# Optimization experiments

Hardware: AMD Instinct MI355X
Metric: run time of the kernel (lower is better)

## Reference

```python
import jax, jax.numpy as jnp
import numpy as np

NUM_C = 1000
B, L = 8, 1024
D, H, NB, DFF = 512, 8, 4, 2048
DK = D // H
EPS = 1e-5


def _ln(x, s, b):
    mu = jnp.mean(x, axis=-1, keepdims=True)
    var = jnp.mean((x - mu) ** 2, axis=-1, keepdims=True)
    return (x - mu) * jax.lax.rsqrt(var + EPS) * s + b


def setup_inputs() -> dict:
    key = jax.random.key(0)
    ks = iter(jax.random.split(key, 64))

    def nrm(shape, scale=0.02):
        return jax.random.normal(next(ks), shape, dtype=jnp.float32) * scale

    inp = {
        "q": jax.random.randint(next(ks), (B, L), 0, NUM_C),
        "r": jax.random.randint(next(ks), (B, L), 0, 2),
        # embeddings
        "ctx_emb": nrm((NUM_C * 2, D)),
        "val_emb": nrm((NUM_C * 2, D)),
        "skill_emb": nrm((NUM_C, D)),
        "pos_emb": nrm((L, D)),
        # attention projections, stacked over blocks
        "Wq": nrm((NB, D, D)), "bq": jnp.zeros((NB, D)),
        "Wk": nrm((NB, D, D)), "bk": jnp.zeros((NB, D)),
        "Wv": nrm((NB, D, D)), "bv": jnp.zeros((NB, D)),
        "Wo": nrm((NB, D, D)), "bo": jnp.zeros((NB, D)),
        # layer norms (ctx / val streams, pre- and post-FFN)
        "ln1c_s": jnp.ones((NB, D)), "ln1c_b": jnp.zeros((NB, D)),
        "ln1v_s": jnp.ones((NB, D)), "ln1v_b": jnp.zeros((NB, D)),
        "ln2c_s": jnp.ones((NB, D)), "ln2c_b": jnp.zeros((NB, D)),
        "ln2v_s": jnp.ones((NB, D)), "ln2v_b": jnp.zeros((NB, D)),
        # FFNs
        "fc1c_W": nrm((NB, D, DFF)), "fc1c_b": jnp.zeros((NB, DFF)),
        "fc2c_W": nrm((NB, DFF, D)), "fc2c_b": jnp.zeros((NB, D)),
        "fc1v_W": nrm((NB, D, DFF)), "fc1v_b": jnp.zeros((NB, DFF)),
        "fc2v_W": nrm((NB, DFF, D)), "fc2v_b": jnp.zeros((NB, D)),
        # prediction head: [3D -> DFF -> 256 -> 1]
        "hW1": nrm((3 * D, DFF)), "hb1": jnp.zeros((DFF,)),
        "hW2": nrm((DFF, 256)), "hb2": jnp.zeros((256,)),
        "hW3": nrm((256, 1)), "hb3": jnp.zeros((1,)),
    }
    return inp


def reference(q, r, ctx_emb, val_emb, skill_emb, pos_emb,
              Wq, bq, Wk, bk, Wv, bv, Wo, bo,
              ln1c_s, ln1c_b, ln1v_s, ln1v_b,
              ln2c_s, ln2c_b, ln2v_s, ln2v_b,
              fc1c_W, fc1c_b, fc2c_W, fc2c_b,
              fc1v_W, fc1v_b, fc2v_W, fc2v_b,
              hW1, hb1, hW2, hb2, hW3, hb3):
    inter = q + NUM_C * r                       # [B, L] interaction ids
    pos = pos_emb[None, :L, :]
    ctx = ctx_emb[inter] + pos                  # [B, L, D]
    val = val_emb[inter] + pos                  # [B, L, D]
    causal = jnp.tril(jnp.ones((L, L), dtype=bool))
    scale = 1.0 / (DK ** 0.5)

    for i in range(NB):
        # dual-stream MHA: Q,K from ctx; V from val
        Q = (ctx @ Wq[i] + bq[i]).reshape(B, L, H, DK)
        K = (ctx @ Wk[i] + bk[i]).reshape(B, L, H, DK)
        V = (val @ Wv[i] + bv[i]).reshape(B, L, H, DK)
        # fp32 scores (as in torch source), mask==0 -> -inf, softmax
        scores = jnp.einsum('bqhd,bkhd->bhqk', Q.astype(jnp.float32),
                            K.astype(jnp.float32)) * scale
        scores = jnp.where(causal, scores, -jnp.inf)
        attn = jax.nn.softmax(scores, axis=-1)  # dropout = identity (eval)
        out = jnp.einsum('bhqk,bkhd->bqhd', attn, V).reshape(B, L, D)
        out = out @ Wo[i] + bo[i]
        # shared attn output added to both streams, separate norms
        ctx = _ln(ctx + out, ln1c_s[i], ln1c_b[i])
        val = _ln(val + out, ln1v_s[i], ln1v_b[i])
        # dual FFNs
        f_ctx = jax.nn.relu(ctx @ fc1c_W[i] + fc1c_b[i]) @ fc2c_W[i] + fc2c_b[i]
        ctx = _ln(ctx + f_ctx, ln2c_s[i], ln2c_b[i])
        f_val = jax.nn.relu(val @ fc1v_W[i] + fc1v_b[i]) @ fc2v_W[i] + fc2v_b[i]
        val = _ln(val + f_val, ln2v_s[i], ln2v_b[i])

    feat = jnp.concatenate([ctx, val, skill_emb[q]], axis=-1)  # [B, L, 3D]
    h = jax.nn.relu(feat @ hW1 + hb1)
    h = jax.nn.relu(h @ hW2 + hb2)
    logits = (h @ hW3 + hb3)[..., 0]
    return jax.nn.sigmoid(logits)               # [B, L] p(correct)
```

## Files before the change

### kernel.cpp

```cpp
#include <hip/hip_runtime.h>
#include <hip/hip_bf16.h>
#include <math.h>

#define TOK 8192
#define DM 512
#define NH 8
#define DKH 64
#define DFFN 2048
#define SEQ 1024
#define NBLK 4
#define NUMC 1000

typedef __attribute__((ext_vector_type(8))) short bf16x8;
typedef __attribute__((ext_vector_type(4))) float f32x4;
typedef __attribute__((ext_vector_type(4))) ushort u16x4;
typedef __hip_bfloat16 bf16;

__device__ __forceinline__ void gload_lds16(const ushort* g, ushort* l) {
    __builtin_amdgcn_global_load_lds(
        (const __attribute__((address_space(1))) void*)g,
        (__attribute__((address_space(3))) void*)l, 16, 0, 0);
}

__global__ __launch_bounds__(256) void embed_kernel(
    const int* __restrict__ q, const int* __restrict__ r,
    const float* __restrict__ ctx_emb, const float* __restrict__ val_emb,
    const float* __restrict__ pos_emb,
    float* __restrict__ ctx32, float* __restrict__ val32,
    bf16* __restrict__ ctx16, bf16* __restrict__ val16)
{
    const int t = blockIdx.x;
    const int inter = q[t] + NUMC * r[t];
    const int l = t & (SEQ - 1);
    const float* ce = ctx_emb + (size_t)inter * DM;
    const float* ve = val_emb + (size_t)inter * DM;
    const float* pe = pos_emb + (size_t)l * DM;
    const size_t o = (size_t)t * DM;
    for (int d = threadIdx.x; d < DM; d += 256) {
        float p = pe[d];
        float c = ce[d] + p;
        float v = ve[d] + p;
        ctx32[o + d] = c; val32[o + d] = v;
        ctx16[o + d] = __float2bfloat16(c);
        val16[o + d] = __float2bfloat16(v);
    }
}

__global__ __launch_bounds__(256) void transpose_kernel(
    const float* __restrict__ src, bf16* __restrict__ dst,
    int K, int N, long sb, long db)
{
    __shared__ float t[32][33];
    src += (long)blockIdx.z * sb;
    dst += (long)blockIdx.z * db;
    const int n0 = blockIdx.x * 32;
    const int k0 = blockIdx.y * 32;
    const int tx = threadIdx.x;
    const int ty = threadIdx.y;
    for (int i = ty; i < 32; i += 8) t[i][tx] = src[(size_t)(k0 + i) * N + n0 + tx];
    __syncthreads();
    for (int i = ty; i < 32; i += 8)
        dst[(size_t)(n0 + i) * K + k0 + tx] = __float2bfloat16(t[tx][i]);
}

template<int BN, bool OUTBF16>
__global__ __launch_bounds__(256, 3) void mfma_gemm(
    const ushort* __restrict__ A, const ushort* __restrict__ Bt,
    const float* __restrict__ bias1, const float* __restrict__ bias2, int split,
    void* __restrict__ Cv, int N, int K, int relu, int vtmode,
    const ushort* __restrict__ A1, const ushort* __restrict__ Bt1,
    const float* __restrict__ bias1_1, void* __restrict__ Cv1)
{
    if (blockIdx.z) { A = A1; Bt = Bt1; bias1 = bias1_1; Cv = Cv1; }
    constexpr int MI = (BN == 128) ? 4 : 2;
    constexpr int BR = BN / 32;
    __shared__ ushort As[128 * 64];
    __shared__ ushort Bs[BN * 64];
    const int tid = threadIdx.x;
    const int wave = tid >> 6;
    const int lane = tid & 63;
    const int ln = lane & 15;
    const int kq = lane >> 4;
    const int nx = gridDim.x;
    const int lin = blockIdx.x + nx * blockIdx.y;
    const int loc = lin >> 3;
    const int mdiv = loc / nx;
    const int bm = ((lin & 7) + 8 * mdiv) * 128;
    const int bn = (loc - mdiv * nx) * BN;
    const int wr = (BN == 128) ? (wave >> 1) * 64 : wave * 32;
    const int wc = (BN == 128) ? (wave & 1) * 64 : 0;

    const int trow = tid >> 3;
    const int gcb = (tid & 7) ^ (trow & 7);
    const ushort* Ab = A + (size_t)(bm + trow) * K + gcb * 8;
    const ushort* Bb = Bt + (size_t)(bn + trow) * K + gcb * 8;
    ushort* AsW = As + wave * 512;
    ushort* BsW = Bs + wave * 512;

    f32x4 acc[MI][4];
#pragma unroll
    for (int i = 0; i < MI; ++i)
#pragma unroll
        for (int j = 0; j < 4; ++j) acc[i][j] = (f32x4){0.f, 0.f, 0.f, 0.f};

    for (int k0 = 0; k0 < K; k0 += 64) {
        __syncthreads();
#pragma unroll
        for (int p = 0; p < 4; ++p)
            gload_lds16(Ab + (size_t)32 * p * K + k0, AsW + p * 2048);
#pragma unroll
        for (int p = 0; p < BR; ++p)
            gload_lds16(Bb + (size_t)32 * p * K + k0, BsW + p * 2048);
        __syncthreads();
#pragma unroll
        for (int half = 0; half < 2; ++half) {
            const int cb = ((half * 4 + kq) ^ (ln & 7)) * 8;
            bf16x8 bfr[4];
#pragma unroll
            for (int j = 0; j < 4; ++j)
                bfr[j] = *(const bf16x8*)&Bs[(wc + j * 16 + ln) * 64 + cb];
#pragma unroll
            for (int i = 0; i < MI; ++i) {
                const bf16x8 af = *(const bf16x8*)&As[(wr + i * 16 + ln) * 64 + cb];
#pragma unroll
                for (int j = 0; j < 4; ++j)
                    acc[i][j] = __builtin_amdgcn_mfma_f32_16x16x32_bf16(af, bfr[j], acc[i][j], 0, 0, 0);
            }
        }
    }

#pragma unroll
    for (int i = 0; i < MI; ++i) {
        const int rowb = bm + wr + i * 16 + kq * 4;
#pragma unroll
        for (int j = 0; j < 4; ++j) {
            const int colg = bn + wc + j * 16 + ln;
            const float bv = (colg < split) ? bias1[colg] : bias2[colg - split];
            if (vtmode) {
                union { u16x4 v; ushort u[4]; } pk;
#pragma unroll
                for (int rr = 0; rr < 4; ++rr) {
                    float v = acc[i][j][rr] + bv;
                    bf16 t = __float2bfloat16(v);
                    pk.u[rr] = *(ushort*)&t;
                }
                *(u16x4*)((ushort*)Cv + ((size_t)(rowb >> 10) * 512 + colg) * 1024 + (rowb & 1023)) = pk.v;
            } else {
#pragma unroll
                for (int rr = 0; rr < 4; ++rr) {
                    float v = acc[i][j][rr] + bv;
                    if (relu) v = fmaxf(v, 0.f);
                    if (OUTBF16)
                        ((bf16*)Cv)[(size_t)(rowb + rr) * N + colg] = __float2bfloat16(v);
                    else
                        ((float*)Cv)[(size_t)(rowb + rr) * N + colg] = v;
                }
            }
        }
    }
}

__global__ __launch_bounds__(256) void attn_kernel(
    const bf16* __restrict__ QK, const bf16* __restrict__ Vt,
    bf16* __restrict__ Og)
{
    __shared__ ushort Qs[64 * 64];
    __shared__ ushort Ks[64 * 64];
    __shared__ ushort Vs[64 * 64];
    __shared__ ushort Ps[4 * 16 * 68];

    const int tid = threadIdx.x;
    const int wave = tid >> 6, lane = tid & 63;
    const int ln = lane & 15, kq = lane >> 4;
    const int lin = blockIdx.x + 16 * blockIdx.y;
    const int loc = lin >> 3;
    const int qt = loc & 15;
    const int bh = (lin & 7) + 8 * (loc >> 4);
    const int b = bh >> 3, h = bh & 7;

    const int srow = tid >> 3;
    const int sgcb = (tid & 7) ^ (srow & 7);
    const ushort* gQ = (const ushort*)QK + (size_t)(b * SEQ + qt * 64 + srow) * 1024 + h * 64 + sgcb * 8;
    const ushort* gK = (const ushort*)QK + (size_t)(b * SEQ + srow) * 1024 + 512 + h * 64 + sgcb * 8;
    const ushort* gV = (const ushort*)Vt + (size_t)(bh * 64 + srow) * 1024 + sgcb * 8;
    ushort* QsW = Qs + wave * 512;
    ushort* KsW = Ks + wave * 512;
    ushort* VsW = Vs + wave * 512;

    gload_lds16(gQ, QsW);
    gload_lds16(gQ + 32 * 1024, QsW + 2048);

    float rs[4];
    f32x4 oacc[4];
#pragma unroll
    for (int r = 0; r < 4; ++r) { rs[r] = 0.f; oacc[r] = (f32x4){0.f, 0.f, 0.f, 0.f}; }
    const float sc2 = 0.125f * 1.4426950408889634f;

    const int cb0 = (kq ^ (ln & 7)) * 8;
    const int cb1 = ((4 + kq) ^ (ln & 7)) * 8;

    for (int kt = 0; kt <= qt; ++kt) {
        __syncthreads();
        gload_lds16(gK + (size_t)kt * 64 * 1024, KsW);
        gload_lds16(gK + (size_t)(kt * 64 + 32) * 1024, KsW + 2048);
        gload_lds16(gV + kt * 64, VsW);
        gload_lds16(gV + 32 * 1024 + kt * 64, VsW + 2048);
        __syncthreads();

        const bf16x8 aq0 = *(const bf16x8*)&Qs[(wave * 16 + ln) * 64 + cb0];
        const bf16x8 aq1 = *(const bf16x8*)&Qs[(wave * 16 + ln) * 64 + cb1];
        f32x4 s[4];
#pragma unroll
        for (int c = 0; c < 4; ++c) {
            const bf16x8 bk0 = *(const bf16x8*)&Ks[(c * 16 + ln) * 64 + cb0];
            const bf16x8 bk1 = *(const bf16x8*)&Ks[(c * 16 + ln) * 64 + cb1];
            s[c] = (f32x4){0.f, 0.f, 0.f, 0.f};
            s[c] = __builtin_amdgcn_mfma_f32_16x16x32_bf16(aq0, bk0, s[c], 0, 0, 0);
            s[c] = __builtin_amdgcn_mfma_f32_16x16x32_bf16(aq1, bk1, s[c], 0, 0, 0);
        }
        if (kt == qt) {
#pragma unroll
            for (int c = 0; c < 4; ++c)
#pragma unroll
                for (int r = 0; r < 4; ++r) {
                    const int qg = wave * 16 + kq * 4 + r;
                    const int jg = c * 16 + ln;
                    const float pv = (jg <= qg) ? exp2f(s[c][r] * sc2) : 0.f;
                    rs[r] += pv;
                    *(bf16*)&Ps[wave * 1088 + (kq * 4 + r) * 68 + c * 16 + ln] = __float2bfloat16(pv);
                }
        } else {
#pragma unroll
            for (int c = 0; c < 4; ++c)
#pragma unroll
                for (int r = 0; r < 4; ++r) {
                    const float pv = exp2f(s[c][r] * sc2);
                    rs[r] += pv;
                    *(bf16*)&Ps[wave * 1088 + (kq * 4 + r) * 68 + c * 16 + ln] = __float2bfloat16(pv);
                }
        }
        const bf16x8 ap0 = *(const bf16x8*)&Ps[wave * 1088 + ln * 68 + kq * 8];
        const bf16x8 ap1 = *(const bf16x8*)&Ps[wave * 1088 + ln * 68 + 32 + kq * 8];
#pragma unroll
        for (int c2 = 0; c2 < 4; ++c2) {
            const bf16x8 bv0 = *(const bf16x8*)&Vs[(c2 * 16 + ln) * 64 + cb0];
            const bf16x8 bv1 = *(const bf16x8*)&Vs[(c2 * 16 + ln) * 64 + cb1];
            oacc[c2] = __builtin_amdgcn_mfma_f32_16x16x32_bf16(ap0, bv0, oacc[c2], 0, 0, 0);
            oacc[c2] = __builtin_amdgcn_mfma_f32_16x16x32_bf16(ap1, bv1, oacc[c2], 0, 0, 0);
        }
    }
    float inv[4];
#pragma unroll
    for (int r = 0; r < 4; ++r) {
        float v = rs[r];
        v += __shfl_xor(v, 1);
        v += __shfl_xor(v, 2);
        v += __shfl_xor(v, 4);
        v += __shfl_xor(v, 8);
        inv[r] = 1.f / v;
    }
#pragma unroll
    for (int c2 = 0; c2 < 4; ++c2)
#pragma unroll
        for (int r = 0; r < 4; ++r)
            Og[(size_t)(b * SEQ + qt * 64 + wave * 16 + kq * 4 + r) * 512 + h * 64 + c2 * 16 + ln]
                = __float2bfloat16(oacc[c2][r] * inv[r]);
}

__global__ __launch_bounds__(256) void lnp_kernel(
    const float* __restrict__ x0, const bf16* __restrict__ r0, const float* __restrict__ s0,
    const float* __restrict__ b0, float* __restrict__ of0, bf16* __restrict__ oh0,
    const float* __restrict__ x1, const bf16* __restrict__ r1, const float* __restrict__ s1,
    const float* __restrict__ b1, float* __restrict__ of1, bf16* __restrict__ oh1)
{
    const float* x = x0; const bf16* res = r0; const float* s = s0; const float* bb = b0;
    float* of = of0; bf16* oh = oh0;
    if (blockIdx.y) { x = x1; res = r1; s = s1; bb = b1; of = of1; oh = oh1; }
    __shared__ float w1[4], w2[4];
    const size_t o = (size_t)blockIdx.x * DM;
    const int i0 = threadIdx.x, i1 = threadIdx.x + 256;
    const float v0 = x[o + i0] + __bfloat162float(res[o + i0]);
    const float v1 = x[o + i1] + __bfloat162float(res[o + i1]);
    float sum = v0 + v1;
#pragma unroll
    for (int off = 32; off; off >>= 1) sum += __shfl_down(sum, off);
    if ((threadIdx.x & 63) == 0) w1[threadIdx.x >> 6] = sum;
    __syncthreads();
    const float mu = (w1[0] + w1[1] + w1[2] + w1[3]) * (1.f / DM);
    const float d0 = v0 - mu, d1 = v1 - mu;
    float vs = d0 * d0 + d1 * d1;
#pragma unroll
    for (int off = 32; off; off >>= 1) vs += __shfl_down(vs, off);
    if ((threadIdx.x & 63) == 0) w2[threadIdx.x >> 6] = vs;
    __syncthreads();
    const float rstd = rsqrtf((w2[0] + w2[1] + w2[2] + w2[3]) * (1.f / DM) + 1e-5f);
    const float o0 = d0 * rstd * s[i0] + bb[i0];
    const float o1 = d1 * rstd * s[i1] + bb[i1];
    of[o + i0] = o0; of[o + i1] = o1;
    oh[o + i0] = __float2bfloat16(o0);
    oh[o + i1] = __float2bfloat16(o1);
}

__global__ __launch_bounds__(256) void gather_kernel(
    const bf16* __restrict__ ctx16, const bf16* __restrict__ val16,
    const float* __restrict__ skill, const int* __restrict__ q,
    bf16* __restrict__ feat)
{
    const int t = blockIdx.x;
    const float* sp = skill + (size_t)q[t] * DM;
    const bf16* cp = ctx16 + (size_t)t * DM;
    const bf16* vp = val16 + (size_t)t * DM;
    bf16* fp = feat + (size_t)t * (3 * DM);
    for (int d = threadIdx.x; d < DM; d += 256) {
        fp[d] = cp[d];
        fp[DM + d] = vp[d];
        fp[2 * DM + d] = __float2bfloat16(sp[d]);
    }
}

__global__ __launch_bounds__(256) void logits_kernel(
    const float* __restrict__ h2, const float* __restrict__ w,
    const float* __restrict__ bptr, float* __restrict__ out)
{
    __shared__ float w1[4];
    const int t = blockIdx.x;
    float sum = h2[(size_t)t * 256 + threadIdx.x] * w[threadIdx.x];
#pragma unroll
    for (int off = 32; off; off >>= 1) sum += __shfl_down(sum, off);
    if ((threadIdx.x & 63) == 0) w1[threadIdx.x >> 6] = sum;
    __syncthreads();
    if (threadIdx.x == 0) {
        const float logit = w1[0] + w1[1] + w1[2] + w1[3] + bptr[0];
        out[t] = 1.f / (1.f + __expf(-logit));
    }
}

extern "C" void kernel_launch(void* const* d_in, const int* in_sizes, int n_in,
                              void* d_out, int out_size, void* d_ws, size_t ws_size,
                              hipStream_t stream)
{
    const int*   q         = (const int*)d_in[0];
    const int*   r         = (const int*)d_in[1];
    const float* ctx_emb   = (const float*)d_in[2];
    const float* val_emb   = (const float*)d_in[3];
    const float* skill_emb = (const float*)d_in[4];
    const float* pos_emb   = (const float*)d_in[5];
    const float* Wq = (const float*)d_in[6];
    const float* bq = (const float*)d_in[7];
    const float* Wk = (const float*)d_in[8];
    const float* bk = (const float*)d_in[9];
    const float* Wv = (const float*)d_in[10];
    const float* bv = (const float*)d_in[11];
    const float* Wo = (const float*)d_in[12];
    const float* bo = (const float*)d_in[13];
    const float* ln1c_s = (const float*)d_in[14];
    const float* ln1c_b = (const float*)d_in[15];
    const float* ln1v_s = (const float*)d_in[16];
    const float* ln1v_b = (const float*)d_in[17];
    const float* ln2c_s = (const float*)d_in[18];
    const float* ln2c_b = (const float*)d_in[19];
    const float* ln2v_s = (const float*)d_in[20];
    const float* ln2v_b = (const float*)d_in[21];
    const float* fc1c_W = (const float*)d_in[22];
    const float* fc1c_b = (const float*)d_in[23];
    const float* fc2c_W = (const float*)d_in[24];
    const float* fc2c_b = (const float*)d_in[25];
    const float* fc1v_W = (const float*)d_in[26];
    const float* fc1v_b = (const float*)d_in[27];
    const float* fc2v_W = (const float*)d_in[28];
    const float* fc2v_b = (const float*)d_in[29];
    const float* hW1 = (const float*)d_in[30];
    const float* hb1 = (const float*)d_in[31];
    const float* hW2 = (const float*)d_in[32];
    const float* hb2 = (const float*)d_in[33];
    const float* hW3 = (const float*)d_in[34];
    const float* hb3 = (const float*)d_in[35];
    float* out = (float*)d_out;

    char* p = (char*)d_ws;
    auto alloc = [&](size_t bytes) { char* ret = p; p += bytes; return ret; };
    float* ctx32 = (float*)alloc(16777216);
    float* val32 = (float*)alloc(16777216);
    bf16*  ob16c = (bf16*)alloc(8388608);
    bf16*  ob16v = (bf16*)alloc(8388608);
    bf16*  ctx16 = (bf16*)alloc(8388608);
    bf16*  val16 = (bf16*)alloc(8388608);
    bf16*  qk16  = (bf16*)alloc(16777216);
    bf16*  v16pad= (bf16*)alloc(8388608);
    bf16*  vt16  = (bf16*)alloc(8388608);
    bf16*  att16 = (bf16*)alloc(8388608);
    bf16*  mid16c = (bf16*)alloc(33554432);
    bf16*  qkT   = (bf16*)alloc(4194304);
    bf16*  vT    = (bf16*)alloc(2097152);
    bf16*  oT    = (bf16*)alloc(2097152);
    bf16*  fc1cT = (bf16*)alloc(8388608);
    bf16*  fc2cT = (bf16*)alloc(8388608);
    bf16*  fc1vT = (bf16*)alloc(8388608);
    bf16*  fc2vT = (bf16*)alloc(8388608);
    bf16*  hW1T  = (bf16*)alloc(6291456);
    bf16*  hW2T  = (bf16*)alloc(1048576);
    (void)v16pad;
    bf16*  mid16v = qk16;
    bf16*  feat16 = qk16;
    float* h2     = (float*)vt16;

    const dim3 tb(32, 8);
    transpose_kernel<<<dim3(16, 16, 4), tb, 0, stream>>>(Wq, qkT,          512, 512, 262144, 524288);
    transpose_kernel<<<dim3(16, 16, 4), tb, 0, stream>>>(Wk, qkT + 262144, 512, 512, 262144, 524288);
    transpose_kernel<<<dim3(16, 16, 4), tb, 0, stream>>>(Wv, vT, 512, 512, 262144, 262144);
    transpose_kernel<<<dim3(16, 16, 4), tb, 0, stream>>>(Wo, oT, 512, 512, 262144, 262144);
    transpose_kernel<<<dim3(64, 16, 4), tb, 0, stream>>>(fc1c_W, fc1cT, 512, 2048, 1048576, 1048576);
    transpose_kernel<<<dim3(16, 64, 4), tb, 0, stream>>>(fc2c_W, fc2cT, 2048, 512, 1048576, 1048576);
    transpose_kernel<<<dim3(64, 16, 4), tb, 0, stream>>>(fc1v_W, fc1vT, 512, 2048, 1048576, 1048576);
    transpose_kernel<<<dim3(16, 64, 4), tb, 0, stream>>>(fc2v_W, fc2vT, 2048, 512, 1048576, 1048576);
    transpose_kernel<<<dim3(64, 48, 1), tb, 0, stream>>>(hW1, hW1T, 1536, 2048, 0, 0);
    transpose_kernel<<<dim3(8, 64, 1),  tb, 0, stream>>>(hW2, hW2T, 2048, 256, 0, 0);

    embed_kernel<<<TOK, 256, 0, stream>>>(q, r, ctx_emb, val_emb, pos_emb,
                                          ctx32, val32, ctx16, val16);

    for (int i = 0; i < NBLK; ++i) {
        mfma_gemm<128, true><<<dim3(8, 64), 256, 0, stream>>>(
            (const ushort*)ctx16, (const ushort*)(qkT + (size_t)i * 524288),
            bq + i * DM, bk + i * DM, 512, qk16, 1024, 512, 0, 0,
            nullptr, nullptr, nullptr, nullptr);
        mfma_gemm<64, true><<<dim3(8, 64), 256, 0, stream>>>(
            (const ushort*)val16, (const ushort*)(vT + (size_t)i * 262144),
            bv + i * DM, nullptr, 1 << 30, vt16, 512, 512, 0, 1,
            nullptr, nullptr, nullptr, nullptr);
        attn_kernel<<<dim3(16, 64), 256, 0, stream>>>(qk16, vt16, att16);
        mfma_gemm<64, true><<<dim3(8, 64), 256, 0, stream>>>(
            (const ushort*)att16, (const ushort*)(oT + (size_t)i * 262144),
            bo + i * DM, nullptr, 1 << 30, ob16c, 512, 512, 0, 0,
            nullptr, nullptr, nullptr, nullptr);
        lnp_kernel<<<dim3(TOK, 2), 256, 0, stream>>>(
            ctx32, ob16c, ln1c_s + i * DM, ln1c_b + i * DM, ctx32, ctx16,
            val32, ob16c, ln1v_s + i * DM, ln1v_b + i * DM, val32, val16);
        mfma_gemm<128, true><<<dim3(16, 64, 2), 256, 0, stream>>>(
            (const ushort*)ctx16, (const ushort*)(fc1cT + (size_t)i * 1048576),
            fc1c_b + i * DFFN, nullptr, 1 << 30, mid16c, 2048, 512, 1, 0,
            (const ushort*)val16, (const ushort*)(fc1vT + (size_t)i * 1048576),
            fc1v_b + i * DFFN, mid16v);
        mfma_gemm<128, true><<<dim3(4, 64, 2), 256, 0, stream>>>(
            (const ushort*)mid16c, (const ushort*)(fc2cT + (size_t)i * 1048576),
            fc2c_b + i * DM, nullptr, 1 << 30, ob16c, 512, 2048, 0, 0,
            (const ushort*)mid16v, (const ushort*)(fc2vT + (size_t)i * 1048576),
            fc2v_b + i * DM, ob16v);
        lnp_kernel<<<dim3(TOK, 2), 256, 0, stream>>>(
            ctx32, ob16c, ln2c_s + i * DM, ln2c_b + i * DM, ctx32, ctx16,
            val32, ob16v, ln2v_s + i * DM, ln2v_b + i * DM, val32, val16);
    }

    gather_kernel<<<TOK, 256, 0, stream>>>(ctx16, val16, skill_emb, q, feat16);
    mfma_gemm<128, true><<<dim3(16, 64), 256, 0, stream>>>(
        (const ushort*)feat16, (const ushort*)hW1T, hb1, nullptr, 1 << 30, mid16c, 2048, 1536, 1, 0,
        nullptr, nullptr, nullptr, nullptr);
    mfma_gemm<64, false><<<dim3(4, 64), 256, 0, stream>>>(
        (const ushort*)mid16c, (const ushort*)hW2T, hb2, nullptr, 1 << 30, h2, 256, 2048, 1, 0,
        nullptr, nullptr, nullptr, nullptr);
    logits_kernel<<<TOK, 256, 0, stream>>>(h2, hW3, hb3, out);
}
```

Baseline: 1.120 ms.

## Add 256x256-tile double-buffered MFMA GEMM for FC1 and head GEMMs

Introduces a new 512-thread GEMM kernel with 256x256 output tiles, double-buffered LDS staging via global_load_lds, XOR-swizzled LDS layout, grouped block ordering and setprio around MFMA bursts. It replaces the 128-tile GEMM for the dual FC1 projections and the first head layer. Larger tiles raise arithmetic intensity and cut global reloads, and overlapping the next tile load with compute hides latency. In exchange it uses more LDS per block and fewer blocks, which lowers occupancy and wave balance.

```diff
diff --git a/kernel.cpp b/kernel.cpp
--- a/kernel.cpp
+++ b/kernel.cpp
@@ -20,6 +20,12 @@
     __builtin_amdgcn_global_load_lds(
         (const __attribute__((address_space(1))) void*)g,
         (__attribute__((address_space(3))) void*)l, 16, 0, 0);
+}
+
+__device__ __forceinline__ void wgbar() {
+    asm volatile("" ::: "memory");
+    __builtin_amdgcn_s_barrier();
+    asm volatile("" ::: "memory");
 }
 
 __global__ __launch_bounds__(256) void embed_kernel(
@@ -155,6 +161,111 @@
                     else
                         ((float*)Cv)[(size_t)(rowb + rr) * N + colg] = v;
                 }
+            }
+        }
+    }
+}
+
+__device__ __forceinline__ void stage256(const ushort* Ag, const ushort* Bg,
+                                         ushort* AsD, ushort* BsD, int K, int kk)
+{
+#pragma unroll
+    for (int p = 0; p < 4; ++p)
+        gload_lds16(Ag + (size_t)(64 * p) * K + kk, AsD + p * 4096);
+#pragma unroll
+    for (int p = 0; p < 4; ++p)
+        gload_lds16(Bg + (size_t)(64 * p) * K + kk, BsD + p * 4096);
+}
+
+__global__ __launch_bounds__(512, 2) void mfma_gemm256(
+    const ushort* __restrict__ A, const ushort* __restrict__ Bt,
+    const float* __restrict__ bias, bf16* __restrict__ C, int N, int K, int relu,
+    const ushort* __restrict__ A1, const ushort* __restrict__ Bt1,
+    const float* __restrict__ bias1, bf16* __restrict__ C1)
+{
+    if (blockIdx.z) { A = A1; Bt = Bt1; bias = bias1; C = C1; }
+    __shared__ ushort As[2 * 16384];
+    __shared__ ushort Bs[2 * 16384];
+    const int tid = threadIdx.x;
+    const int wave = tid >> 6, lane = tid & 63;
+    const int ln = lane & 15, kq = lane >> 4;
+    const int wr = wave >> 2;
+    const int wc = wave & 3;
+
+    const int nx = gridDim.x;
+    const int lin = blockIdx.x + nx * blockIdx.y;
+    const int loc = lin >> 3;
+    const int mdiv = loc / nx;
+    const int bm = ((lin & 7) + 8 * mdiv) * 256;
+    const int bn = (loc - mdiv * nx) * 256;
+
+    const int srow = tid >> 3;
+    const int sgcb = (tid & 7) ^ (srow & 7);
+    const ushort* Ag = A + (size_t)(bm + srow) * K + sgcb * 8;
+    const ushort* Bg = Bt + (size_t)(bn + srow) * K + sgcb * 8;
+    const int wofs = wave * 512;
+
+    f32x4 acc[8][4];
+#pragma unroll
+    for (int i = 0; i < 8; ++i)
+#pragma unroll
+        for (int j = 0; j < 4; ++j) acc[i][j] = (f32x4){0.f, 0.f, 0.f, 0.f};
+
+    const int NT = K >> 6;
+    stage256(Ag, Bg, As + wofs, Bs + wofs, K, 0);
+
+    for (int t = 0; t < NT; ++t) {
+        const int b = t & 1;
+        const int k0 = t << 6;
+        if (t + 1 < NT) {
+            stage256(Ag, Bg, As + (b ^ 1) * 16384 + wofs, Bs + (b ^ 1) * 16384 + wofs, K, k0 + 64);
+            asm volatile("s_waitcnt vmcnt(8)" ::: "memory");
+        } else {
+            asm volatile("s_waitcnt vmcnt(0)" ::: "memory");
+        }
+        wgbar();
+
+        const ushort* Asb = As + b * 16384;
+        const ushort* Bsb = Bs + b * 16384;
+        bf16x8 bf[4][2];
+#pragma unroll
+        for (int j = 0; j < 4; ++j)
+#pragma unroll
+            for (int h = 0; h < 2; ++h)
+                bf[j][h] = *(const bf16x8*)&Bsb[(wc * 64 + j * 16 + ln) * 64 + (((h * 4 + kq) ^ (ln & 7)) * 8)];
+#pragma unroll
+        for (int q = 0; q < 4; ++q) {
+            bf16x8 af0[2], af1[2];
+#pragma unroll
+            for (int h = 0; h < 2; ++h) {
+                af0[h] = *(const bf16x8*)&Asb[(wr * 128 + (2 * q) * 16 + ln) * 64 + (((h * 4 + kq) ^ (ln & 7)) * 8)];
+                af1[h] = *(const bf16x8*)&Asb[(wr * 128 + (2 * q + 1) * 16 + ln) * 64 + (((h * 4 + kq) ^ (ln & 7)) * 8)];
+            }
+            __builtin_amdgcn_s_setprio(1);
+#pragma unroll
+            for (int h = 0; h < 2; ++h)
+#pragma unroll
+                for (int j = 0; j < 4; ++j) {
+                    acc[2 * q][j]     = __builtin_amdgcn_mfma_f32_16x16x32_bf16(af0[h], bf[j][h], acc[2 * q][j], 0, 0, 0);
+                    acc[2 * q + 1][j] = __builtin_amdgcn_mfma_f32_16x16x32_bf16(af1[h], bf[j][h], acc[2 * q + 1][j], 0, 0, 0);
+                }
+            __builtin_amdgcn_s_setprio(0);
+            wgbar();
+        }
+    }
+
+#pragma unroll
+    for (int i = 0; i < 8; ++i) {
+        const int gr = bm + wr * 128 + i * 16 + kq * 4;
+#pragma unroll
+        for (int j = 0; j < 4; ++j) {
+            const int gc = bn + wc * 64 + j * 16 + ln;
+            const float bv = bias[gc];
+#pragma unroll
+            for (int rr = 0; rr < 4; ++rr) {
+                float v = acc[i][j][rr] + bv;
+                if (relu) v = fmaxf(v, 0.f);
+                C[(size_t)(gr + rr) * N + gc] = __float2bfloat16(v);
             }
         }
     }
@@ -436,9 +547,9 @@
         lnp_kernel<<<dim3(TOK, 2), 256, 0, stream>>>(
             ctx32, ob16c, ln1c_s + i * DM, ln1c_b + i * DM, ctx32, ctx16,
             val32, ob16c, ln1v_s + i * DM, ln1v_b + i * DM, val32, val16);
-        mfma_gemm<128, true><<<dim3(16, 64, 2), 256, 0, stream>>>(
+        mfma_gemm256<<<dim3(8, 32, 2), 512, 0, stream>>>(
             (const ushort*)ctx16, (const ushort*)(fc1cT + (size_t)i * 1048576),
-            fc1c_b + i * DFFN, nullptr, 1 << 30, mid16c, 2048, 512, 1, 0,
+            fc1c_b + i * DFFN, mid16c, 2048, 512, 1,
             (const ushort*)val16, (const ushort*)(fc1vT + (size_t)i * 1048576),
             fc1v_b + i * DFFN, mid16v);
         mfma_gemm<128, true><<<dim3(4, 64, 2), 256, 0, stream>>>(
@@ -452,8 +563,8 @@
     }
 
     gather_kernel<<<TOK, 256, 0, stream>>>(ctx16, val16, skill_emb, q, feat16);
-    mfma_gemm<128, true><<<dim3(16, 64), 256, 0, stream>>>(
-        (const ushort*)feat16, (const ushort*)hW1T, hb1, nullptr, 1 << 30, mid16c, 2048, 1536, 1, 0,
+    mfma_gemm256<<<dim3(8, 32), 512, 0, stream>>>(
+        (const ushort*)feat16, (const ushort*)hW1T, hb1, mid16c, 2048, 1536, 1,
         nullptr, nullptr, nullptr, nullptr);
     mfma_gemm<64, false><<<dim3(4, 64), 256, 0, stream>>>(
         (const ushort*)mid16c, (const ushort*)hW2T, hb2, nullptr, 1 << 30, h2, 256, 2048, 1, 0,
```

After: 1.140 ms. Within noise of the previous version (+1.8%).

## Double-buffer K/V tiles in attention kernel with async prefetch

Applied to the files above, without the earlier changes.

Double-buffers the K and V shared-memory tiles in the causal attention kernel. The next tile is prefetched with direct global-to-LDS loads while the current one is computed, and explicit vmcnt waits plus raw barriers replace the two __syncthreads per iteration. The aim is to hide global-load latency behind MFMA work. It also raises wave priority around the MFMA sections, and it doubles K/V shared-memory use, which may reduce occupancy.

```diff
diff --git a/kernel.cpp b/kernel.cpp
--- a/kernel.cpp
+++ b/kernel.cpp
@@ -20,6 +20,12 @@
     __builtin_amdgcn_global_load_lds(
         (const __attribute__((address_space(1))) void*)g,
         (__attribute__((address_space(3))) void*)l, 16, 0, 0);
+}
+
+__device__ __forceinline__ void wgbar() {
+    asm volatile("" ::: "memory");
+    __builtin_amdgcn_s_barrier();
+    asm volatile("" ::: "memory");
 }
 
 __global__ __launch_bounds__(256) void embed_kernel(
@@ -165,8 +171,8 @@
     bf16* __restrict__ Og)
 {
     __shared__ ushort Qs[64 * 64];
-    __shared__ ushort Ks[64 * 64];
-    __shared__ ushort Vs[64 * 64];
+    __shared__ ushort Ks[2][64 * 64];
+    __shared__ ushort Vs[2][64 * 64];
     __shared__ ushort Ps[4 * 16 * 68];
 
     const int tid = threadIdx.x;
@@ -184,12 +190,17 @@
     const ushort* gK = (const ushort*)QK + (size_t)(b * SEQ + srow) * 1024 + 512 + h * 64 + sgcb * 8;
     const ushort* gV = (const ushort*)Vt + (size_t)(bh * 64 + srow) * 1024 + sgcb * 8;
     ushort* QsW = Qs + wave * 512;
-    ushort* KsW = Ks + wave * 512;
-    ushort* VsW = Vs + wave * 512;
 
     gload_lds16(gQ, QsW);
     gload_lds16(gQ + 32 * 1024, QsW + 2048);
 
+    {
+        gload_lds16(gK, Ks[0] + wave * 512);
+        gload_lds16(gK + (size_t)32 * 1024, Ks[0] + 2048 + wave * 512);
+        gload_lds16(gV, Vs[0] + wave * 512);
+        gload_lds16(gV + (size_t)32 * 1024, Vs[0] + 2048 + wave * 512);
+    }
+
     float rs[4];
     f32x4 oacc[4];
 #pragma unroll
@@ -200,24 +211,33 @@
     const int cb1 = ((4 + kq) ^ (ln & 7)) * 8;
 
     for (int kt = 0; kt <= qt; ++kt) {
-        __syncthreads();
-        gload_lds16(gK + (size_t)kt * 64 * 1024, KsW);
-        gload_lds16(gK + (size_t)(kt * 64 + 32) * 1024, KsW + 2048);
-        gload_lds16(gV + kt * 64, VsW);
-        gload_lds16(gV + 32 * 1024 + kt * 64, VsW + 2048);
-        __syncthreads();
+        const int bf = kt & 1;
+        wgbar();
+        if (kt < qt) {
+            const size_t kn = (size_t)(kt + 1) * 64;
+            gload_lds16(gK + kn * 1024, Ks[bf ^ 1] + wave * 512);
+            gload_lds16(gK + (kn + 32) * 1024, Ks[bf ^ 1] + 2048 + wave * 512);
+            gload_lds16(gV + kn, Vs[bf ^ 1] + wave * 512);
+            gload_lds16(gV + (size_t)32 * 1024 + kn, Vs[bf ^ 1] + 2048 + wave * 512);
+            asm volatile("s_waitcnt vmcnt(4)" ::: "memory");
+        } else {
+            asm volatile("s_waitcnt vmcnt(0)" ::: "memory");
+        }
+        wgbar();
 
         const bf16x8 aq0 = *(const bf16x8*)&Qs[(wave * 16 + ln) * 64 + cb0];
         const bf16x8 aq1 = *(const bf16x8*)&Qs[(wave * 16 + ln) * 64 + cb1];
         f32x4 s[4];
+        __builtin_amdgcn_s_setprio(1);
 #pragma unroll
         for (int c = 0; c < 4; ++c) {
-            const bf16x8 bk0 = *(const bf16x8*)&Ks[(c * 16 + ln) * 64 + cb0];
-            const bf16x8 bk1 = *(const bf16x8*)&Ks[(c * 16 + ln) * 64 + cb1];
+            const bf16x8 bk0 = *(const bf16x8*)&Ks[bf][(c * 16 + ln) * 64 + cb0];
+            const bf16x8 bk1 = *(const bf16x8*)&Ks[bf][(c * 16 + ln) * 64 + cb1];
             s[c] = (f32x4){0.f, 0.f, 0.f, 0.f};
             s[c] = __builtin_amdgcn_mfma_f32_16x16x32_bf16(aq0, bk0, s[c], 0, 0, 0);
             s[c] = __builtin_amdgcn_mfma_f32_16x16x32_bf16(aq1, bk1, s[c], 0, 0, 0);
         }
+        __builtin_amdgcn_s_setprio(0);
         if (kt == qt) {
 #pragma unroll
             for (int c = 0; c < 4; ++c)
@@ -241,13 +261,15 @@
         }
         const bf16x8 ap0 = *(const bf16x8*)&Ps[wave * 1088 + ln * 68 + kq * 8];
         const bf16x8 ap1 = *(const bf16x8*)&Ps[wave * 1088 + ln * 68 + 32 + kq * 8];
+        __builtin_amdgcn_s_setprio(1);
 #pragma unroll
         for (int c2 = 0; c2 < 4; ++c2) {
-            const bf16x8 bv0 = *(const bf16x8*)&Vs[(c2 * 16 + ln) * 64 + cb0];
-            const bf16x8 bv1 = *(const bf16x8*)&Vs[(c2 * 16 + ln) * 64 + cb1];
+            const bf16x8 bv0 = *(const bf16x8*)&Vs[bf][(c2 * 16 + ln) * 64 + cb0];
+            const bf16x8 bv1 = *(const bf16x8*)&Vs[bf][(c2 * 16 + ln) * 64 + cb1];
             oacc[c2] = __builtin_amdgcn_mfma_f32_16x16x32_bf16(ap0, bv0, oacc[c2], 0, 0, 0);
             oacc[c2] = __builtin_amdgcn_mfma_f32_16x16x32_bf16(ap1, bv1, oacc[c2], 0, 0, 0);
         }
+        __builtin_amdgcn_s_setprio(0);
     }
     float inv[4];
 #pragma unroll
```

Result: slower. 1.154 ms (+3.0%).
